# Kernel optimization log

Measured on AMD Instinct MI355X. Metric: run time of the kernel, lower is better.

Reference implementation:

```python
import jax, jax.numpy as jnp
import numpy as np

D = 1024      # model_dimension
H = 16        # num_heads
HD = D // H   # head_dimension (shared K/V head dim)
B, S = 2, 2048


def setup_inputs() -> dict:
    key = jax.random.key(0)
    ks = jax.random.split(key, 11)
    s = 0.02
    return {
        "q": jax.random.normal(ks[0], (B, S, D), jnp.float32),
        "k": jax.random.normal(ks[1], (B, S, D), jnp.float32),
        "v": jax.random.normal(ks[2], (B, S, D), jnp.float32),
        "Wq": jax.random.normal(ks[3], (D, D), jnp.float32) * s,
        "bq": jnp.zeros((D,), jnp.float32),
        "Wk": jax.random.normal(ks[4], (D, HD), jnp.float32) * s,
        "bk": jnp.zeros((HD,), jnp.float32),
        "Wv": jax.random.normal(ks[5], (D, HD), jnp.float32) * s,
        "bv": jnp.zeros((HD,), jnp.float32),
        "Wo": jax.random.normal(ks[6], (D, D), jnp.float32) * s,
        "bo": jnp.zeros((D,), jnp.float32),
    }


def reference(q, k, v, Wq, bq, Wk, bk, Wv, bv, Wo, bo):
    Bsz, Sq, Dm = q.shape
    # Q projection + split into heads: (B, H, Sq, HD)
    qh = (q @ Wq + bq).reshape(Bsz, Sq, H, HD).transpose(0, 2, 1, 3)
    # Shared single K/V head: (B, Sk, HD)
    kh = k @ Wk + bk
    vh = v @ Wv + bv
    # Scores (B, H, Sq, Sk), scaled then clamped as in the original
    scores = jnp.einsum('bhqd,bkd->bhqk', qh, kh) / jnp.sqrt(jnp.float32(HD))
    scores = jnp.clip(scores, -1e6, 1e6)
    attn = jax.nn.softmax(scores, axis=-1)
    out = jnp.einsum('bhqk,bkd->bhqd', attn, vh)
    out = out.transpose(0, 2, 1, 3).reshape(Bsz, Sq, Dm)
    return out @ Wo + bo
```

## Files before the change

kernel.cpp:

```cpp
#include <hip/hip_runtime.h>
#include <cstdint>
#include <cstddef>

typedef unsigned short u16;
typedef uint32_t u32;
typedef __bf16 bf16x8 __attribute__((ext_vector_type(8)));
typedef float  f32x4  __attribute__((ext_vector_type(4)));
typedef u16    u16x4  __attribute__((ext_vector_type(4)));
typedef u32    u32x4  __attribute__((ext_vector_type(4)));

#define DEV static __device__ __forceinline__
#define MFMA16(a, b, c) __builtin_amdgcn_mfma_f32_16x16x32_bf16(a, b, c, 0, 0, 0)

DEV u16 f2bf(float x) {
  unsigned u = __float_as_uint(x);
  u += 0x7fffu + ((u >> 16) & 1u);
  return (u16)(u >> 16);
}

DEV u32 cvt_pk_bf16(float lo, float hi) {
  u32 r;
  asm("v_cvt_pk_bf16_f32 %0, %1, %2" : "=v"(r) : "v"(lo), "v"(hi));
  return r;
}

DEV void gload_lds16(const void* g, void* l) {
  __builtin_amdgcn_global_load_lds(
      (__attribute__((address_space(1))) void*)(void*)g,
      (__attribute__((address_space(3))) void*)l, 16, 0, 0);
}

__global__ void k_transpose4(const float* __restrict__ Wq, u16* __restrict__ WqT,
                             const float* __restrict__ Wo, u16* __restrict__ WoT,
                             const float* __restrict__ Wk, u16* __restrict__ WkT,
                             const float* __restrict__ Wv, u16* __restrict__ WvT) {
  __shared__ float tile[32][33];
  const int z = blockIdx.z;
  const int C = z < 2 ? 1024 : 64;
  constexpr int R = 1024;
  if (blockIdx.x * 32 >= C) return;
  const float* in = z == 0 ? Wq : z == 1 ? Wo : z == 2 ? Wk : Wv;
  u16* out = z == 0 ? WqT : z == 1 ? WoT : z == 2 ? WkT : WvT;
  int bx = blockIdx.x * 32, by = blockIdx.y * 32;
  int tx = threadIdx.x, ty = threadIdx.y;
#pragma unroll
  for (int j = 0; j < 4; ++j)
    tile[ty + j * 8][tx] = in[(size_t)(by + ty + j * 8) * C + bx + tx];
  __syncthreads();
#pragma unroll
  for (int j = 0; j < 4; ++j)
    out[(size_t)(bx + ty + j * 8) * R + by + tx] = f2bf(tile[tx][ty + j * 8]);
}

template <bool OUT_BF16, bool A_FP32>
__global__ __launch_bounds__(512) void k_gemm128(const void* __restrict__ Ap, const u16* __restrict__ Bt,
                                                 const float* __restrict__ bias, void* __restrict__ Cout,
                                                 int M, int N, int K, float scale) {
  __shared__ u16 As[2][128 * 32];
  __shared__ u16 Bs[2][128 * 32];
  const int tid = threadIdx.x, lane = tid & 63, wid = tid >> 6;
  const int s = blockIdx.x;
  const int xr = s & 7, t = s >> 3;
  const int bx = t & 7;
  const int by = (t >> 3) * 8 + xr;
  const int brow = by * 128, bcol = bx * 128;
  const int wr = (wid >> 2) * 64, wc = (wid & 3) * 32;

  const int e0 = wid * 512 + lane * 8;
  const u16* b0 = Bt + (size_t)(bcol + (e0 >> 5)) * K + (e0 & 31);
  const u16* a0bf = A_FP32 ? nullptr : (const u16*)Ap + (size_t)(brow + (e0 >> 5)) * K + (e0 & 31);
  const float* a0f = A_FP32 ? (const float*)Ap + (size_t)(brow + (tid >> 2)) * K + (tid & 3) * 8 : nullptr;

  f32x4 ra0, ra1;
  auto LOADA = [&](int k0) {
    ra0 = *(const f32x4*)(a0f + k0);
    ra1 = *(const f32x4*)(a0f + k0 + 4);
  };
  auto WRITEA = [&](int buf) {
    u32x4 w;
    w[0] = cvt_pk_bf16(ra0[0], ra0[1]);
    w[1] = cvt_pk_bf16(ra0[2], ra0[3]);
    w[2] = cvt_pk_bf16(ra1[0], ra1[1]);
    w[3] = cvt_pk_bf16(ra1[2], ra1[3]);
    *(u32x4*)&As[buf][tid * 8] = w;
  };

  f32x4 acc[4][2] = {};
  const int NK = K / 32;
  if constexpr (A_FP32) {
    LOADA(0);
    gload_lds16(b0, &Bs[0][wid * 512]);
    WRITEA(0);
    LOADA(32);
    asm volatile("s_waitcnt lgkmcnt(0)" ::: "memory");
  } else {
    gload_lds16(a0bf, &As[0][wid * 512]);
    gload_lds16(b0, &Bs[0][wid * 512]);
  }
#pragma unroll 1
  for (int ks = 0; ks < NK; ++ks) {
    if (ks + 1 < NK) {
      if constexpr (A_FP32) {
        gload_lds16(b0 + (ks + 1) * 32, &Bs[(ks + 1) & 1][wid * 512]);
        asm volatile("s_waitcnt vmcnt(3)\n\ts_barrier" ::: "memory");
      } else {
        gload_lds16(a0bf + (ks + 1) * 32, &As[(ks + 1) & 1][wid * 512]);
        gload_lds16(b0 + (ks + 1) * 32, &Bs[(ks + 1) & 1][wid * 512]);
        asm volatile("s_waitcnt vmcnt(2)\n\ts_barrier" ::: "memory");
      }
    } else {
      asm volatile("s_waitcnt vmcnt(0)\n\ts_barrier" ::: "memory");
    }
    __builtin_amdgcn_sched_barrier(0);

    const u16* Ab = &As[ks & 1][0];
    const u16* Bb = &Bs[ks & 1][0];
    const int lr = lane & 15, lk = (lane >> 4) * 8;
    bf16x8 af[4], bfr[2];
#pragma unroll
    for (int m = 0; m < 4; ++m) af[m] = *(const bf16x8*)&Ab[(wr + m * 16 + lr) * 32 + lk];
#pragma unroll
    for (int n = 0; n < 2; ++n) bfr[n] = *(const bf16x8*)&Bb[(wc + n * 16 + lr) * 32 + lk];
    __builtin_amdgcn_s_setprio(1);
#pragma unroll
    for (int m = 0; m < 4; ++m)
#pragma unroll
      for (int n = 0; n < 2; ++n) acc[m][n] = MFMA16(af[m], bfr[n], acc[m][n]);
    __builtin_amdgcn_s_setprio(0);

    if constexpr (A_FP32) {
      if (ks + 1 < NK) {
        WRITEA((ks + 1) & 1);
        if (ks + 2 < NK) LOADA((ks + 2) * 32);
      }
      asm volatile("s_waitcnt lgkmcnt(0)\n\ts_barrier" ::: "memory");
    } else {
      asm volatile("s_barrier" ::: "memory");
    }
  }

  const int lr = lane & 15, lg = lane >> 4;
#pragma unroll
  for (int m = 0; m < 4; ++m)
#pragma unroll
    for (int n = 0; n < 2; ++n) {
      const int col = bcol + wc + n * 16 + lr;
      const float bv = bias ? bias[col] : 0.f;
#pragma unroll
      for (int r = 0; r < 4; ++r) {
        const int row = brow + wr + m * 16 + lg * 4 + r;
        float val = (acc[m][n][r] + bv) * scale;
        if constexpr (OUT_BF16) ((u16*)Cout)[(size_t)row * N + col] = f2bf(val);
        else ((float*)Cout)[(size_t)row * N + col] = val;
      }
    }
}

__global__ __launch_bounds__(256) void k_gemm64(const float* __restrict__ A0, const float* __restrict__ A1,
                                                const u16* __restrict__ Bt0, const u16* __restrict__ Bt1,
                                                const float* __restrict__ bias0, const float* __restrict__ bias1,
                                                u16* __restrict__ C0, u16* __restrict__ C1, int K) {
  __shared__ u16 As[2][64 * 32];
  __shared__ u16 Bs[2][64 * 32];
  const int sel = blockIdx.y;
  const float* Af = sel ? A1 : A0;
  const u16* Bt = sel ? Bt1 : Bt0;
  const float* bias = sel ? bias1 : bias0;
  const int tid = threadIdx.x, lane = tid & 63, wid = tid >> 6;
  const int brow = blockIdx.x * 64;
  const int e0 = wid * 512 + lane * 8;
  const u16* b0 = Bt + (size_t)(e0 >> 5) * K + (e0 & 31);
  const float* a0f = Af + (size_t)(brow + (tid >> 2)) * K + (tid & 3) * 8;

  f32x4 ra0, ra1;
  auto LOADA = [&](int k0) {
    ra0 = *(const f32x4*)(a0f + k0);
    ra1 = *(const f32x4*)(a0f + k0 + 4);
  };
  auto WRITEA = [&](int buf) {
    u32x4 w;
    w[0] = cvt_pk_bf16(ra0[0], ra0[1]);
    w[1] = cvt_pk_bf16(ra0[2], ra0[3]);
    w[2] = cvt_pk_bf16(ra1[0], ra1[1]);
    w[3] = cvt_pk_bf16(ra1[2], ra1[3]);
    *(u32x4*)&As[buf][tid * 8] = w;
  };

  f32x4 acc[4] = {};
  const int NK = K / 32;
  LOADA(0);
  gload_lds16(b0, &Bs[0][wid * 512]);
  WRITEA(0);
  LOADA(32);
  asm volatile("s_waitcnt lgkmcnt(0)" ::: "memory");
#pragma unroll 1
  for (int ks = 0; ks < NK; ++ks) {
    if (ks + 1 < NK) {
      gload_lds16(b0 + (ks + 1) * 32, &Bs[(ks + 1) & 1][wid * 512]);
      asm volatile("s_waitcnt vmcnt(3)\n\ts_barrier" ::: "memory");
    } else {
      asm volatile("s_waitcnt vmcnt(0)\n\ts_barrier" ::: "memory");
    }
    __builtin_amdgcn_sched_barrier(0);

    const u16* Ab = &As[ks & 1][0];
    const u16* Bb = &Bs[ks & 1][0];
    const int lr = lane & 15, lk = (lane >> 4) * 8;
    bf16x8 af = *(const bf16x8*)&Ab[(wid * 16 + lr) * 32 + lk];
    __builtin_amdgcn_s_setprio(1);
#pragma unroll
    for (int n = 0; n < 4; ++n) {
      bf16x8 bfr = *(const bf16x8*)&Bb[(n * 16 + lr) * 32 + lk];
      acc[n] = MFMA16(af, bfr, acc[n]);
    }
    __builtin_amdgcn_s_setprio(0);

    if (ks + 1 < NK) {
      WRITEA((ks + 1) & 1);
      if (ks + 2 < NK) LOADA((ks + 2) * 32);
    }
    asm volatile("s_waitcnt lgkmcnt(0)\n\ts_barrier" ::: "memory");
  }

  const int lr = lane & 15, lg = lane >> 4;
#pragma unroll
  for (int n = 0; n < 4; ++n) {
    const int col = n * 16 + lr;
    const float bv = bias[col];
#pragma unroll
    for (int r = 0; r < 4; ++r) {
      const int row = brow + wid * 16 + lg * 4 + r;
      const float val = acc[n][r] + bv;
      if (sel)
        C1[((size_t)(row >> 11) * 64 + col) * 2048 + (row & 2047)] = f2bf(val);
      else
        C0[(size_t)row * 64 + col] = f2bf(val);
    }
  }
}

__global__ __launch_bounds__(512) void k_attn(const float* __restrict__ qsrc, const u16* __restrict__ WqT,
                                              const float* __restrict__ bq,
                                              const u16* __restrict__ Kh, const u16* __restrict__ VhT,
                                              u16* __restrict__ Out) {
  constexpr int S = 2048, D = 1024, NT = 32, K = 1024;
  __shared__ __align__(16) char smem[49152];
  const int tid = threadIdx.x, lane = tid & 63, wid = tid >> 6;
  const int lr = lane & 15, lg = lane >> 4;
  const int q0 = blockIdx.x * 128;
  const int h = blockIdx.y, b = blockIdx.z;

  u16* AsQ = (u16*)smem;
  u16* BsQ = (u16*)(smem + 16384);
  u16* Qlds = (u16*)(smem + 32768);

  const float* a0f = qsrc + (size_t)(b * S + q0 + (tid >> 2)) * K + (tid & 3) * 8;
  const int eB = (wid & 3) * 512 + lane * 8;
  const u16* b0q = WqT + (size_t)(h * 64 + (eB >> 5)) * K + (eB & 31);

  f32x4 ra0, ra1;
  auto LOADA = [&](int k0) {
    ra0 = *(const f32x4*)(a0f + k0);
    ra1 = *(const f32x4*)(a0f + k0 + 4);
  };
  auto WRITEA = [&](int buf) {
    u32x4 w;
    w[0] = cvt_pk_bf16(ra0[0], ra0[1]);
    w[1] = cvt_pk_bf16(ra0[2], ra0[3]);
    w[2] = cvt_pk_bf16(ra1[0], ra1[1]);
    w[3] = cvt_pk_bf16(ra1[2], ra1[3]);
    *(u32x4*)&AsQ[buf * (128 * 32) + tid * 8] = w;
  };

  {
    f32x4 accq[4] = {};
    LOADA(0);
    gload_lds16(b0q, &BsQ[(wid & 3) * 512]);
    WRITEA(0);
    LOADA(32);
    asm volatile("s_waitcnt lgkmcnt(0)" ::: "memory");
#pragma unroll 1
    for (int ks = 0; ks < 32; ++ks) {
      if (ks + 1 < 32) {
        gload_lds16(b0q + (ks + 1) * 32, &BsQ[((ks + 1) & 1) * (64 * 32) + (wid & 3) * 512]);
        asm volatile("s_waitcnt vmcnt(3)\n\ts_barrier" ::: "memory");
      } else {
        asm volatile("s_waitcnt vmcnt(0)\n\ts_barrier" ::: "memory");
      }
      __builtin_amdgcn_sched_barrier(0);

      const u16* Ab = &AsQ[(ks & 1) * (128 * 32)];
      const u16* Bb = &BsQ[(ks & 1) * (64 * 32)];
      const int lk = (lane >> 4) * 8;
      bf16x8 af = *(const bf16x8*)&Ab[(wid * 16 + lr) * 32 + lk];
      __builtin_amdgcn_s_setprio(1);
#pragma unroll
      for (int n = 0; n < 4; ++n) {
        bf16x8 bfr = *(const bf16x8*)&Bb[(n * 16 + lr) * 32 + lk];
        accq[n] = MFMA16(af, bfr, accq[n]);
      }
      __builtin_amdgcn_s_setprio(0);

      if (ks + 1 < 32) {
        WRITEA((ks + 1) & 1);
        if (ks + 2 < 32) LOADA((ks + 2) * 32);
      }
      asm volatile("s_waitcnt lgkmcnt(0)\n\ts_barrier" ::: "memory");
    }
    const float qscale = 0.125f * 1.44269504089f;
#pragma unroll
    for (int n = 0; n < 4; ++n) {
      const float bv = bq[h * 64 + n * 16 + lr];
#pragma unroll
      for (int r = 0; r < 4; ++r)
        Qlds[(wid * 16 + lg * 4 + r) * 64 + n * 16 + lr] = f2bf((accq[n][r] + bv) * qscale);
    }
    asm volatile("s_waitcnt vmcnt(0) lgkmcnt(0)\n\ts_barrier" ::: "memory");
  }

  u16* Ks0 = (u16*)smem;
  u16* Vs0 = (u16*)(smem + 16384);
  u16* Pw = Qlds + wid * (16 * 64);

  bf16x8 qf[2];
#pragma unroll
  for (int kk = 0; kk < 2; ++kk)
    qf[kk] = *(const bf16x8*)&Qlds[(wid * 16 + lr) * 64 + kk * 32 + lg * 8];

  const int r8 = lane >> 3, ssl = (lane & 7) ^ r8;
  const u16* ksrc = Kh + (size_t)(b * S + wid * 8 + r8) * 64 + ssl * 8;
  const u16* vsrc = VhT + (size_t)(b * 64 + wid * 8 + r8) * S + ssl * 8;

  float lsum = 0.f;
  f32x4 o[4] = {};
  const int pswz = (lr & 7) << 3;

  auto STAGE = [&](int buf, int t) {
    gload_lds16(ksrc + (size_t)(t * 64) * 64, &Ks0[buf * (64 * 64) + (wid * 8) * 64]);
    gload_lds16(vsrc + t * 64, &Vs0[buf * (64 * 64) + (wid * 8) * 64]);
  };

  STAGE(0, 0);
#pragma unroll 1
  for (int t = 0; t < NT; ++t) {
    if (t + 1 < NT) {
      STAGE((t + 1) & 1, t + 1);
      asm volatile("s_waitcnt vmcnt(2)\n\ts_barrier" ::: "memory");
    } else {
      asm volatile("s_waitcnt vmcnt(0)\n\ts_barrier" ::: "memory");
    }
    __builtin_amdgcn_sched_barrier(0);

    const u16* Kb = &Ks0[(t & 1) * (64 * 64)];
    const u16* Vb = &Vs0[(t & 1) * (64 * 64)];

    f32x4 z[4] = {};
    __builtin_amdgcn_s_setprio(1);
#pragma unroll
    for (int kk = 0; kk < 2; ++kk)
#pragma unroll
      for (int ct = 0; ct < 4; ++ct) {
        const int row = ct * 16 + lr;
        bf16x8 kf = *(const bf16x8*)&Kb[row * 64 + (((kk * 4 + lg) ^ (row & 7)) << 3)];
        z[ct] = MFMA16(kf, qf[kk], z[ct]);
      }
    __builtin_amdgcn_s_setprio(0);

    float s = 0.f;
#pragma unroll
    for (int ct = 0; ct < 4; ++ct) {
      const float p0 = __builtin_amdgcn_exp2f(z[ct][0]);
      const float p1 = __builtin_amdgcn_exp2f(z[ct][1]);
      const float p2 = __builtin_amdgcn_exp2f(z[ct][2]);
      const float p3 = __builtin_amdgcn_exp2f(z[ct][3]);
      s += (p0 + p1) + (p2 + p3);
      uint2 pk;
      pk.x = cvt_pk_bf16(p0, p1);
      pk.y = cvt_pk_bf16(p2, p3);
      *(uint2*)&Pw[lr * 64 + ((ct * 16 + lg * 4) ^ pswz)] = pk;
    }
    lsum += s;

#pragma unroll
    for (int kk = 0; kk < 2; ++kk) {
      bf16x8 pa = *(const bf16x8*)&Pw[lr * 64 + ((kk * 32 + lg * 8) ^ pswz)];
      __builtin_amdgcn_s_setprio(1);
#pragma unroll
      for (int nt = 0; nt < 4; ++nt) {
        const int row = nt * 16 + lr;
        bf16x8 vf = *(const bf16x8*)&Vb[row * 64 + (((kk * 4 + lg) ^ (row & 7)) << 3)];
        o[nt] = MFMA16(pa, vf, o[nt]);
      }
      __builtin_amdgcn_s_setprio(0);
    }
    asm volatile("s_barrier" ::: "memory");
  }

  lsum += __shfl_xor(lsum, 16);
  lsum += __shfl_xor(lsum, 32);
  const float linv = 1.f / lsum;
#pragma unroll
  for (int r = 0; r < 4; ++r) {
    const float li = __shfl(linv, (lane & 48) | (lg * 4 + r));
    const size_t row = (size_t)(b * S + q0 + wid * 16 + lg * 4 + r);
#pragma unroll
    for (int nt = 0; nt < 4; ++nt)
      Out[row * D + h * 64 + nt * 16 + lr] = f2bf(o[nt][r] * li);
  }
}

extern "C" void kernel_launch(void* const* d_in, const int* in_sizes, int n_in,
                              void* d_out, int out_size, void* d_ws, size_t ws_size,
                              hipStream_t stream) {
  const float* q  = (const float*)d_in[0];
  const float* k  = (const float*)d_in[1];
  const float* v  = (const float*)d_in[2];
  const float* Wq = (const float*)d_in[3];
  const float* bq = (const float*)d_in[4];
  const float* Wk = (const float*)d_in[5];
  const float* bk = (const float*)d_in[6];
  const float* Wv = (const float*)d_in[7];
  const float* bv = (const float*)d_in[8];
  const float* Wo = (const float*)d_in[9];
  const float* bo = (const float*)d_in[10];
  float* out = (float*)d_out;

  constexpr int B = 2, S = 2048, D = 1024, H = 16, HDc = 64;
  constexpr int M = B * S;

  char* ws = (char*)d_ws;
  size_t off = 0;
  auto alloc = [&](size_t bytes) { char* p = ws + off; off += bytes; return p; };
  u16* WqT  = (u16*)alloc((size_t)D * D * 2);
  u16* WkvT = (u16*)alloc((size_t)2 * HDc * D * 2);
  u16* WoT  = (u16*)alloc((size_t)D * D * 2);
  u16* Kh   = (u16*)alloc((size_t)M * HDc * 2);
  u16* VhT  = (u16*)alloc((size_t)M * HDc * 2);
  u16* AO   = (u16*)alloc((size_t)M * D * 2);
  u16* WkT = WkvT;
  u16* WvT = WkvT + (size_t)HDc * D;

  k_transpose4<<<dim3(32, 32, 4), dim3(32, 8), 0, stream>>>(Wq, WqT, Wo, WoT, Wk, WkT, Wv, WvT);
  k_gemm64<<<dim3(M / 64, 2), 256, 0, stream>>>(k, v, WkT, WvT, bk, bv, Kh, VhT, D);
  k_attn<<<dim3(S / 128, H, B), 512, 0, stream>>>(q, WqT, bq, Kh, VhT, AO);
  k_gemm128<false, false><<<dim3((M / 128) * (D / 128)), 512, 0, stream>>>(AO, WoT, bo, out, M, D, D, 1.0f);
}
```

Baseline: 114.5 us.

## Widen fused Q-projection K-step to 64 with swizzled LDS and head-major grid

The Q projection inside the attention kernel now uses a K-step of 64 instead of 32, halving the number of barrier-separated iterations. A+B tiles in LDS use an XOR swizzle to avoid bank conflicts, and B is now loaded by all 8 waves. The grid is reordered so heads vary fastest, letting blocks that share the same q rows run together and reuse them in L2. Larger tiles use more LDS and registers per iteration, and BsQ now overlaps Qlds, so the two buffers must not be live at the same time.

```diff
diff --git a/kernel.cpp b/kernel.cpp
--- a/kernel.cpp
+++ b/kernel.cpp
@@ -247,63 +247,80 @@
   __shared__ __align__(16) char smem[49152];
   const int tid = threadIdx.x, lane = tid & 63, wid = tid >> 6;
   const int lr = lane & 15, lg = lane >> 4;
-  const int q0 = blockIdx.x * 128;
-  const int h = blockIdx.y, b = blockIdx.z;
+  const int h = blockIdx.x;
+  const int q0 = blockIdx.y * 128;
+  const int b = blockIdx.z;
 
   u16* AsQ = (u16*)smem;
-  u16* BsQ = (u16*)(smem + 16384);
+  u16* BsQ = (u16*)(smem + 32768);
   u16* Qlds = (u16*)(smem + 32768);
 
-  const float* a0f = qsrc + (size_t)(b * S + q0 + (tid >> 2)) * K + (tid & 3) * 8;
-  const int eB = (wid & 3) * 512 + lane * 8;
-  const u16* b0q = WqT + (size_t)(h * 64 + (eB >> 5)) * K + (eB & 31);
-
-  f32x4 ra0, ra1;
+  const int arow = tid >> 2, aq = tid & 3;
+  const float* a0f = qsrc + (size_t)(b * S + q0 + arow) * K + aq * 16;
+  const int bsrc_chunk = (tid & 7) ^ ((tid >> 3) & 7);
+  const u16* b0q = WqT + (size_t)(h * 64 + (tid >> 3)) * K + bsrc_chunk * 8;
+
+  f32x4 ra0, ra1, ra2, ra3;
   auto LOADA = [&](int k0) {
     ra0 = *(const f32x4*)(a0f + k0);
     ra1 = *(const f32x4*)(a0f + k0 + 4);
+    ra2 = *(const f32x4*)(a0f + k0 + 8);
+    ra3 = *(const f32x4*)(a0f + k0 + 12);
   };
   auto WRITEA = [&](int buf) {
-    u32x4 w;
-    w[0] = cvt_pk_bf16(ra0[0], ra0[1]);
-    w[1] = cvt_pk_bf16(ra0[2], ra0[3]);
-    w[2] = cvt_pk_bf16(ra1[0], ra1[1]);
-    w[3] = cvt_pk_bf16(ra1[2], ra1[3]);
-    *(u32x4*)&AsQ[buf * (128 * 32) + tid * 8] = w;
+    u32x4 w0, w1;
+    w0[0] = cvt_pk_bf16(ra0[0], ra0[1]);
+    w0[1] = cvt_pk_bf16(ra0[2], ra0[3]);
+    w0[2] = cvt_pk_bf16(ra1[0], ra1[1]);
+    w0[3] = cvt_pk_bf16(ra1[2], ra1[3]);
+    w1[0] = cvt_pk_bf16(ra2[0], ra2[1]);
+    w1[1] = cvt_pk_bf16(ra2[2], ra2[3]);
+    w1[2] = cvt_pk_bf16(ra3[0], ra3[1]);
+    w1[3] = cvt_pk_bf16(ra3[2], ra3[3]);
+    char* base = (char*)AsQ + buf * 16384 + arow * 128;
+    *(u32x4*)(base + (((aq * 2 + 0) ^ (arow & 7)) << 4)) = w0;
+    *(u32x4*)(base + (((aq * 2 + 1) ^ (arow & 7)) << 4)) = w1;
   };
 
   {
     f32x4 accq[4] = {};
     LOADA(0);
-    gload_lds16(b0q, &BsQ[(wid & 3) * 512]);
+    gload_lds16(b0q, BsQ + wid * 512);
     WRITEA(0);
-    LOADA(32);
+    LOADA(64);
     asm volatile("s_waitcnt lgkmcnt(0)" ::: "memory");
 #pragma unroll 1
-    for (int ks = 0; ks < 32; ++ks) {
-      if (ks + 1 < 32) {
-        gload_lds16(b0q + (ks + 1) * 32, &BsQ[((ks + 1) & 1) * (64 * 32) + (wid & 3) * 512]);
-        asm volatile("s_waitcnt vmcnt(3)\n\ts_barrier" ::: "memory");
+    for (int ks = 0; ks < 16; ++ks) {
+      if (ks + 1 < 16) {
+        gload_lds16(b0q + (ks + 1) * 64, BsQ + ((ks + 1) & 1) * 4096 + wid * 512);
+        asm volatile("s_waitcnt vmcnt(5)\n\ts_barrier" ::: "memory");
       } else {
         asm volatile("s_waitcnt vmcnt(0)\n\ts_barrier" ::: "memory");
       }
       __builtin_amdgcn_sched_barrier(0);
 
-      const u16* Ab = &AsQ[(ks & 1) * (128 * 32)];
-      const u16* Bb = &BsQ[(ks & 1) * (64 * 32)];
-      const int lk = (lane >> 4) * 8;
-      bf16x8 af = *(const bf16x8*)&Ab[(wid * 16 + lr) * 32 + lk];
+      const char* Ab = (const char*)AsQ + (ks & 1) * 16384;
+      const char* Bb = (const char*)BsQ + (ks & 1) * 8192;
+      bf16x8 af[2], bfr;
+#pragma unroll
+      for (int kk = 0; kk < 2; ++kk) {
+        const int row = wid * 16 + lr;
+        af[kk] = *(const bf16x8*)(Ab + row * 128 + (((kk * 4 + lg) ^ (row & 7)) << 4));
+      }
       __builtin_amdgcn_s_setprio(1);
 #pragma unroll
-      for (int n = 0; n < 4; ++n) {
-        bf16x8 bfr = *(const bf16x8*)&Bb[(n * 16 + lr) * 32 + lk];
-        accq[n] = MFMA16(af, bfr, accq[n]);
-      }
+      for (int kk = 0; kk < 2; ++kk)
+#pragma unroll
+        for (int n = 0; n < 4; ++n) {
+          const int row = n * 16 + lr;
+          bfr = *(const bf16x8*)(Bb + row * 128 + (((kk * 4 + lg) ^ (row & 7)) << 4));
+          accq[n] = MFMA16(af[kk], bfr, accq[n]);
+        }
       __builtin_amdgcn_s_setprio(0);
 
-      if (ks + 1 < 32) {
+      if (ks + 1 < 16) {
         WRITEA((ks + 1) & 1);
-        if (ks + 2 < 32) LOADA((ks + 2) * 32);
+        if (ks + 2 < 16) LOADA((ks + 2) * 64);
       }
       asm volatile("s_waitcnt lgkmcnt(0)\n\ts_barrier" ::: "memory");
     }
@@ -315,7 +332,7 @@
       for (int r = 0; r < 4; ++r)
         Qlds[(wid * 16 + lg * 4 + r) * 64 + n * 16 + lr] = f2bf((accq[n][r] + bv) * qscale);
     }
-    asm volatile("s_waitcnt vmcnt(0) lgkmcnt(0)\n\ts_barrier" ::: "memory");
+    asm volatile("s_waitcnt lgkmcnt(0)\n\ts_barrier" ::: "memory");
   }
 
   u16* Ks0 = (u16*)smem;
@@ -442,6 +459,6 @@
 
   k_transpose4<<<dim3(32, 32, 4), dim3(32, 8), 0, stream>>>(Wq, WqT, Wo, WoT, Wk, WkT, Wv, WvT);
   k_gemm64<<<dim3(M / 64, 2), 256, 0, stream>>>(k, v, WkT, WvT, bk, bv, Kh, VhT, D);
-  k_attn<<<dim3(S / 128, H, B), 512, 0, stream>>>(q, WqT, bq, Kh, VhT, AO);
+  k_attn<<<dim3(H, S / 128, B), 512, 0, stream>>>(q, WqT, bq, Kh, VhT, AO);
   k_gemm128<false, false><<<dim3((M / 128) * (D / 128)), 512, 0, stream>>>(AO, WoT, bo, out, M, D, D, 1.0f);
 }
```

New measurement: 113.4 us. Within noise of the previous version (-0.9%).
